# Performance work log

Hardware: AMD Instinct MI355X
Metric: run time of the kernel (lower is better)

The kernel has to match this reference:

```python
import jax, jax.numpy as jnp
import numpy as np

EPS = 1e-8      # torch CosineSimilarity eps (clamps norms)
GAMMA = 0.5
RANK = 2        # hardcoded in the module; rank-1 = 1 negative per sample


def _cos_dist(a, b):
    # angular distance sqrt(2*(1-cos)) along last dim, torch-style eps on norms
    na = jnp.clip(jnp.linalg.norm(a, axis=-1), EPS)
    nb = jnp.clip(jnp.linalg.norm(b, axis=-1), EPS)
    sim = jnp.sum(a * b, axis=-1) / (na * nb)
    return jnp.sqrt(jnp.maximum(2.0 * (1.0 - sim), 1e-12))


def setup_inputs() -> dict:
    key = jax.random.key(0)
    k1, k2, k3 = jax.random.split(key, 3)
    B, D, V = 4096, 512, 50000
    return {
        "input": jax.random.normal(k1, (B, D), dtype=jnp.float32),
        "target": jax.random.normal(k2, (B, D), dtype=jnp.float32),
        "veclist": jax.random.normal(k3, (V, D), dtype=jnp.float32),
    }


def reference(input, target, veclist):
    B = input.shape[0]
    # distance to the true target per sample: [B]
    d_pos = _cos_dist(input, target)

    # brute-force angular kNN over veclist (replaces the Annoy index):
    # max cosine similarity == min angular distance
    inn = input / jnp.clip(jnp.linalg.norm(input, axis=-1, keepdims=True), EPS)
    vnn = veclist / jnp.clip(jnp.linalg.norm(veclist, axis=-1, keepdims=True), EPS)
    sims = inn @ vnn.T                                # [B, V] -- the big GEMM
    _, top_idx = jax.lax.top_k(sims, RANK)            # [B, 2]

    vec0 = veclist[top_idx[:, 0]]                     # [B, D]
    vec1 = veclist[top_idx[:, 1]]                     # [B, D]
    # skip the neighbor if it is exactly the target vector (original `torch.eq` check)
    eq0 = jnp.all(vec0 == target, axis=-1)            # [B]
    neg = jnp.where(eq0[:, None], vec1, vec0)         # [B, D]

    d_neg = _cos_dist(input, neg)                     # [B]
    # original builds sample_dist of shape [rank]=[2] (gamma_vec bug repeats gamma
    # `rank` times), with both entries identical -> sum of positives = 2*relu(margin)
    margin = GAMMA + d_pos - d_neg                    # [B]
    cost = jnp.sum(RANK * jnp.maximum(margin, 0.0))
    return cost / B
```

## Files before the change

### kernel.cpp

```cpp
#include <hip/hip_runtime.h>
#include <hip/hip_bf16.h>
#include <hip/hip_fp8.h>
#include <math.h>

#define B_ROWS 4096
#define DIMS   512
#define V_ROWS 50000
#define V_PAD  50048
#define NTILES 391
#define NT_PAD 392
#define MTILES 32
#define BKB    128
#define NROWS_ALL 54144
#define EPSF   1e-8f
#define QSCALE 64.0f
#define SCALE1 0x7F7F7F7F

typedef float f32x4 __attribute__((ext_vector_type(4)));
typedef int   i32x4 __attribute__((ext_vector_type(4)));
typedef int   i32x8 __attribute__((ext_vector_type(8)));
typedef unsigned long long u64;

__device__ __forceinline__ unsigned int pk4_fp8(float a, float b, float c, float d) {
#if __has_builtin(__builtin_amdgcn_cvt_pk_fp8_f32)
  int w = __builtin_amdgcn_cvt_pk_fp8_f32(a, b, 0, false);
  w = __builtin_amdgcn_cvt_pk_fp8_f32(c, d, w, true);
  return (unsigned int)w;
#else
  __hip_fp8_e4m3 qa(a), qb(b), qc(c), qd(d);
  return (unsigned int)qa.__x | ((unsigned int)qb.__x << 8) |
         ((unsigned int)qc.__x << 16) | ((unsigned int)qd.__x << 24);
#endif
}

__device__ __forceinline__ void lds_load16(const void* g, void* l) {
  __builtin_amdgcn_global_load_lds(
      (const __attribute__((address_space(1))) void*)g,
      (__attribute__((address_space(3))) void*)l, 16, 0, 0);
}

__device__ __forceinline__ u64 pack_key(float v, int col) {
  unsigned int u = __float_as_uint(v);
  unsigned int s = u ^ ((unsigned int)((int)u >> 31) | 0x80000000u);
  return ((u64)s << 32) | (unsigned int)(~col);
}
__device__ __forceinline__ int key_col(u64 k) {
  return (int)(~(unsigned int)k);
}
__device__ __forceinline__ void kmerge(u64& k0, u64& k1, u64 a0, u64 a1) {
  bool bt = a0 > k0;
  u64 lo = bt ? k0 : a0;
  u64 hi = bt ? a1 : k1;
  k0 = bt ? a0 : k0;
  k1 = hi > lo ? hi : lo;
}

__global__ __launch_bounds__(256)
void normalize_rows_kernel(const float* __restrict__ vsrc, const float* __restrict__ isrc,
                           unsigned char* __restrict__ vdst, unsigned char* __restrict__ idst) {
  const int l = threadIdx.x & 63;
  const int gw = (blockIdx.x * 256 + threadIdx.x) >> 6;
  const int nw = (gridDim.x * 256) >> 6;
  for (int row = gw; row < NROWS_ALL; row += nw) {
    const float* src;
    unsigned char* dst;
    if (row < V_PAD) {
      if (row >= V_ROWS) {
        *(uint2*)&vdst[(size_t)row * DIMS + l * 8] = make_uint2(0u, 0u);
        continue;
      }
      src = vsrc + (size_t)row * DIMS;
      dst = vdst + (size_t)row * DIMS;
    } else {
      src = isrc + (size_t)(row - V_PAD) * DIMS;
      dst = idst + (size_t)(row - V_PAD) * DIMS;
    }
    float4 v0 = ((const float4*)src)[l * 2];
    float4 v1 = ((const float4*)src)[l * 2 + 1];
    float ss = v0.x * v0.x + v0.y * v0.y + v0.z * v0.z + v0.w * v0.w
             + v1.x * v1.x + v1.y * v1.y + v1.z * v1.z + v1.w * v1.w;
    #pragma unroll
    for (int d = 1; d < 64; d <<= 1) ss += __shfl_xor(ss, d);
    float s = QSCALE / fmaxf(sqrtf(ss), EPSF);
    uint2 o;
    o.x = pk4_fp8(v0.x * s, v0.y * s, v0.z * s, v0.w * s);
    o.y = pk4_fp8(v1.x * s, v1.y * s, v1.z * s, v1.w * s);
    *(uint2*)&dst[l * 8] = o;
  }
}

__global__ __launch_bounds__(256, 3)
void gemm_top2_kernel(const unsigned char* __restrict__ A8,
                      const unsigned char* __restrict__ B8,
                      ulonglong2* __restrict__ cands) {
  __shared__ __align__(16) unsigned char smem[2 * 128 * BKB];
  unsigned char* const As = smem;
  unsigned char* const Bs = smem + 128 * BKB;

  const int bid = blockIdx.x;
  const int mt = bid & 31;
  const int nt = bid >> 5;
  const int m0 = mt * 128, n0 = nt * 128;

  const int tid = threadIdx.x;
  const int w = tid >> 6, l = tid & 63;
  const int wr = w >> 1, wc = w & 1;
  const int lq = l >> 4, lr = l & 15;
  const int h = lr & 7;

  const int s0 = ((2 * lq) ^ h) * 16;
  const int s1 = ((2 * lq + 1) ^ h) * 16;

  f32x4 acc[4][4] = {};

  for (int k0 = 0; k0 < DIMS; k0 += BKB) {
    #pragma unroll
    for (int it = 0; it < 4; ++it) {
      const int chunk = it * 256 + w * 64 + l;
      const int row = chunk >> 3, c = chunk & 7;
      const int gc = c ^ (row & 7);
      lds_load16(A8 + (size_t)(m0 + row) * DIMS + k0 + gc * 16,
                 &As[(it * 256 + w * 64) * 16]);
      lds_load16(B8 + (size_t)(n0 + row) * DIMS + k0 + gc * 16,
                 &Bs[(it * 256 + w * 64) * 16]);
    }
    __syncthreads();

    i32x8 bf[4];
    #pragma unroll
    for (int tc = 0; tc < 4; ++tc) {
      const int rb = (wc * 64 + tc * 16 + lr) * BKB;
      i32x4 blo = *(const i32x4*)&Bs[rb + s0];
      i32x4 bhi = *(const i32x4*)&Bs[rb + s1];
      bf[tc] = __builtin_shufflevector(blo, bhi, 0, 1, 2, 3, 4, 5, 6, 7);
    }
    #pragma unroll
    for (int tr = 0; tr < 4; ++tr) {
      const int ra = (wr * 64 + tr * 16 + lr) * BKB;
      i32x4 alo = *(const i32x4*)&As[ra + s0];
      i32x4 ahi = *(const i32x4*)&As[ra + s1];
      i32x8 af = __builtin_shufflevector(alo, ahi, 0, 1, 2, 3, 4, 5, 6, 7);
      #pragma unroll
      for (int tc = 0; tc < 4; ++tc)
        acc[tr][tc] = __builtin_amdgcn_mfma_scale_f32_16x16x128_f8f6f4(
            af, bf[tc], acc[tr][tc],
            0, 0,
            0, SCALE1,
            0, SCALE1);
    }
    __syncthreads();
  }

  ulonglong2 (*ep)[32] = (ulonglong2(*)[32])smem;
  const int colbase = n0 + wc * 64 + lr;

  #pragma unroll
  for (int p = 0; p < 2; ++p) {
    #pragma unroll
    for (int trh = 0; trh < 2; ++trh) {
      const int tr = p * 2 + trh;
      #pragma unroll
      for (int rg = 0; rg < 4; ++rg) {
        u64 kk[4];
        #pragma unroll
        for (int tc = 0; tc < 4; ++tc) {
          const int col = colbase + tc * 16;
          const float v = (col < V_ROWS) ? acc[tr][tc][rg] : -INFINITY;
          kk[tc] = pack_key(v, col);
        }
        const bool s01 = kk[0] > kk[1];
        u64 a0 = s01 ? kk[0] : kk[1], a1 = s01 ? kk[1] : kk[0];
        const bool s23 = kk[2] > kk[3];
        u64 b0 = s23 ? kk[2] : kk[3], b1 = s23 ? kk[3] : kk[2];
        kmerge(a0, a1, b0, b1);
        const int slot = wr * 32 + trh * 16 + lq * 4 + rg;
        ep[slot][(wc * 16 + lr) ^ (slot & 7)] = make_ulonglong2(a0, a1);
      }
    }
    __syncthreads();
    {
      const int ms = tid >> 2, q = tid & 3;
      u64 k0 = 0, k1 = 0;
      #pragma unroll
      for (int k = 0; k < 8; ++k) {
        ulonglong2 e = ep[ms][(q * 8 + k) ^ (ms & 7)];
        kmerge(k0, k1, e.x, e.y);
      }
      #pragma unroll
      for (int d = 1; d < 4; d <<= 1) {
        u64 o0 = __shfl_xor(k0, d), o1 = __shfl_xor(k1, d);
        kmerge(k0, k1, o0, o1);
      }
      if (q == 0) {
        const int row = (ms >> 5) * 64 + p * 32 + (ms & 31);
        cands[(size_t)(m0 + row) * NT_PAD + nt] = make_ulonglong2(k0, k1);
      }
    }
    __syncthreads();
  }
}

__global__ __launch_bounds__(256)
void finalize_kernel(const float* __restrict__ input, const float* __restrict__ target,
                     const float* __restrict__ veclist, const ulonglong2* __restrict__ cands,
                     float* __restrict__ contrib) {
  const int b = blockIdx.x;
  const int t = threadIdx.x;
  __shared__ ulonglong2 wpair[4];
  __shared__ int sidx[2];
  __shared__ float red[4][7];
  __shared__ int reda[4];

  u64 k0 = 0, k1 = 0;
  for (int nt = t; nt < NTILES; nt += 256) {
    ulonglong2 c = cands[(size_t)b * NT_PAD + nt];
    kmerge(k0, k1, c.x, c.y);
  }
  #pragma unroll
  for (int d = 1; d < 64; d <<= 1) {
    u64 o0 = __shfl_xor(k0, d), o1 = __shfl_xor(k1, d);
    kmerge(k0, k1, o0, o1);
  }
  if ((t & 63) == 0) wpair[t >> 6] = make_ulonglong2(k0, k1);
  __syncthreads();
  if (t == 0) {
    u64 m0k = wpair[0].x, m1k = wpair[0].y;
    for (int wd = 1; wd < 4; ++wd) kmerge(m0k, m1k, wpair[wd].x, wpair[wd].y);
    sidx[0] = key_col(m0k);
    sidx[1] = key_col(m1k);
  }
  __syncthreads();
  const int idx0 = sidx[0], idx1 = sidx[1];

  const float2* xin = (const float2*)(input  + (size_t)b * DIMS);
  const float2* xtg = (const float2*)(target + (size_t)b * DIMS);
  const float2* xv0 = (const float2*)(veclist + (size_t)idx0 * DIMS);
  const float2* xv1 = (const float2*)(veclist + (size_t)idx1 * DIMS);
  float2 xi = xin[t], tg = xtg[t], a0 = xv0[t], a1 = xv1[t];
  float s[7];
  s[0] = xi.x * xi.x + xi.y * xi.y;
  s[1] = tg.x * tg.x + tg.y * tg.y;
  s[2] = xi.x * tg.x + xi.y * tg.y;
  s[3] = a0.x * a0.x + a0.y * a0.y;
  s[4] = xi.x * a0.x + xi.y * a0.y;
  s[5] = a1.x * a1.x + a1.y * a1.y;
  s[6] = xi.x * a1.x + xi.y * a1.y;
  bool eq = (a0.x == tg.x) && (a0.y == tg.y);
  int weq = __all(eq);
  #pragma unroll
  for (int k = 0; k < 7; ++k)
    #pragma unroll
    for (int d = 1; d < 64; d <<= 1) s[k] += __shfl_xor(s[k], d);
  if ((t & 63) == 0) {
    #pragma unroll
    for (int k = 0; k < 7; ++k) red[t >> 6][k] = s[k];
    reda[t >> 6] = weq;
  }
  __syncthreads();
  if (t == 0) {
    float r[7];
    #pragma unroll
    for (int k = 0; k < 7; ++k)
      r[k] = red[0][k] + red[1][k] + red[2][k] + red[3][k];
    bool eq0 = reda[0] && reda[1] && reda[2] && reda[3];
    float na  = fmaxf(sqrtf(r[0]), EPSF);
    float ntg = fmaxf(sqrtf(r[1]), EPSF);
    float simp = r[2] / (na * ntg);
    float d_pos = sqrtf(fmaxf(2.0f * (1.0f - simp), 1e-12f));
    float nn = eq0 ? fmaxf(sqrtf(r[5]), EPSF) : fmaxf(sqrtf(r[3]), EPSF);
    float dn = eq0 ? r[6] : r[4];
    float simn = dn / (na * nn);
    float d_neg = sqrtf(fmaxf(2.0f * (1.0f - simn), 1e-12f));
    float margin = 0.5f + d_pos - d_neg;
    contrib[b] = 2.0f * fmaxf(margin, 0.0f) * (1.0f / (float)B_ROWS);
  }
}

__global__ __launch_bounds__(256)
void reduce_kernel(const float* __restrict__ contrib, float* __restrict__ out) {
  const int t = threadIdx.x;
  __shared__ float wsum[4];
  float s = 0.0f;
  for (int i = t; i < B_ROWS; i += 256) s += contrib[i];
  #pragma unroll
  for (int d = 1; d < 64; d <<= 1) s += __shfl_xor(s, d);
  if ((t & 63) == 0) wsum[t >> 6] = s;
  __syncthreads();
  if (t == 0) out[0] = wsum[0] + wsum[1] + wsum[2] + wsum[3];
}

extern "C" void kernel_launch(void* const* d_in, const int* in_sizes, int n_in,
                              void* d_out, int out_size, void* d_ws, size_t ws_size,
                              hipStream_t stream) {
  const float* input   = (const float*)d_in[0];
  const float* target  = (const float*)d_in[1];
  const float* veclist = (const float*)d_in[2];
  float* out = (float*)d_out;
  char* ws = (char*)d_ws;
  unsigned char* vnn = (unsigned char*)ws;
  unsigned char* inn = (unsigned char*)(ws + 25624576);
  ulonglong2* cands = (ulonglong2*)(ws + 27721728);
  float* contrib = (float*)(ws + 53411840);

  normalize_rows_kernel<<<2048, 256, 0, stream>>>(veclist, input, vnn, inn);
  gemm_top2_kernel<<<MTILES * NTILES, 256, 0, stream>>>(inn, vnn, cands);
  finalize_kernel<<<B_ROWS, 256, 0, stream>>>(input, target, veclist, cands, contrib);
  reduce_kernel<<<1, 256, 0, stream>>>(contrib, out);
}
```

Before: 362.6 us.

## Double-buffer LDS in FP8 GEMM with explicit waitcnt pipelining and MFMA priority

Turns the GEMM's K loop (four steps of 128) into a fully unrolled, double-buffered LDS pipeline. The next K-slice's global-to-LDS loads are issued before the current slice is computed, with explicit vmcnt waits and raw barriers replacing __syncthreads. MFMA sections are wrapped in s_setprio so the math gets issue priority. LDS use doubles to 64KB and launch bounds drop to 2 blocks per CU, trading occupancy for overlap. The normalize kernel grid size is also doubled.

New measurement: 362.6 us. Within noise of the previous version (+0.0%).

```diff
diff --git a/kernel.cpp b/kernel.cpp
--- a/kernel.cpp
+++ b/kernel.cpp
@@ -89,13 +89,11 @@
   }
 }
 
-__global__ __launch_bounds__(256, 3)
+__global__ __launch_bounds__(256, 2)
 void gemm_top2_kernel(const unsigned char* __restrict__ A8,
                       const unsigned char* __restrict__ B8,
                       ulonglong2* __restrict__ cands) {
-  __shared__ __align__(16) unsigned char smem[2 * 128 * BKB];
-  unsigned char* const As = smem;
-  unsigned char* const Bs = smem + 128 * BKB;
+  __shared__ __align__(16) unsigned char smem[2 * 2 * 128 * BKB];
 
   const int bid = blockIdx.x;
   const int mt = bid & 31;
@@ -113,43 +111,74 @@
 
   f32x4 acc[4][4] = {};
 
-  for (int k0 = 0; k0 < DIMS; k0 += BKB) {
-    #pragma unroll
-    for (int it = 0; it < 4; ++it) {
-      const int chunk = it * 256 + w * 64 + l;
-      const int row = chunk >> 3, c = chunk & 7;
-      const int gc = c ^ (row & 7);
-      lds_load16(A8 + (size_t)(m0 + row) * DIMS + k0 + gc * 16,
-                 &As[(it * 256 + w * 64) * 16]);
-      lds_load16(B8 + (size_t)(n0 + row) * DIMS + k0 + gc * 16,
-                 &Bs[(it * 256 + w * 64) * 16]);
-    }
-    __syncthreads();
-
-    i32x8 bf[4];
-    #pragma unroll
-    for (int tc = 0; tc < 4; ++tc) {
-      const int rb = (wc * 64 + tc * 16 + lr) * BKB;
-      i32x4 blo = *(const i32x4*)&Bs[rb + s0];
-      i32x4 bhi = *(const i32x4*)&Bs[rb + s1];
-      bf[tc] = __builtin_shufflevector(blo, bhi, 0, 1, 2, 3, 4, 5, 6, 7);
-    }
-    #pragma unroll
-    for (int tr = 0; tr < 4; ++tr) {
-      const int ra = (wr * 64 + tr * 16 + lr) * BKB;
-      i32x4 alo = *(const i32x4*)&As[ra + s0];
-      i32x4 ahi = *(const i32x4*)&As[ra + s1];
-      i32x8 af = __builtin_shufflevector(alo, ahi, 0, 1, 2, 3, 4, 5, 6, 7);
-      #pragma unroll
-      for (int tc = 0; tc < 4; ++tc)
-        acc[tr][tc] = __builtin_amdgcn_mfma_scale_f32_16x16x128_f8f6f4(
-            af, bf[tc], acc[tr][tc],
-            0, 0,
-            0, SCALE1,
-            0, SCALE1);
-    }
-    __syncthreads();
-  }
+#define STAGE(buf, k0)                                                        \
+  {                                                                           \
+    unsigned char* Asb = smem + (buf) * 32768;                                \
+    unsigned char* Bsb = Asb + 16384;                                         \
+    _Pragma("unroll")                                                         \
+    for (int it = 0; it < 4; ++it) {                                          \
+      const int chunk = it * 256 + w * 64 + l;                                \
+      const int row = chunk >> 3, c = chunk & 7;                              \
+      const int gc = c ^ (row & 7);                                           \
+      lds_load16(A8 + (size_t)(m0 + row) * DIMS + (k0) + gc * 16,             \
+                 &Asb[(it * 256 + w * 64) * 16]);                             \
+      lds_load16(B8 + (size_t)(n0 + row) * DIMS + (k0) + gc * 16,             \
+                 &Bsb[(it * 256 + w * 64) * 16]);                             \
+    }                                                                         \
+  }
+
+#define COMPUTE(buf)                                                          \
+  {                                                                           \
+    unsigned char* Asb = smem + (buf) * 32768;                                \
+    unsigned char* Bsb = Asb + 16384;                                         \
+    i32x8 bf[4];                                                              \
+    _Pragma("unroll")                                                         \
+    for (int tc = 0; tc < 4; ++tc) {                                          \
+      const int rb = (wc * 64 + tc * 16 + lr) * BKB;                          \
+      i32x4 blo = *(const i32x4*)&Bsb[rb + s0];                               \
+      i32x4 bhi = *(const i32x4*)&Bsb[rb + s1];                               \
+      bf[tc] = __builtin_shufflevector(blo, bhi, 0, 1, 2, 3, 4, 5, 6, 7);     \
+    }                                                                         \
+    _Pragma("unroll")                                                         \
+    for (int tr = 0; tr < 4; ++tr) {                                          \
+      const int ra = (wr * 64 + tr * 16 + lr) * BKB;                          \
+      i32x4 alo = *(const i32x4*)&Asb[ra + s0];                               \
+      i32x4 ahi = *(const i32x4*)&Asb[ra + s1];                               \
+      i32x8 af = __builtin_shufflevector(alo, ahi, 0, 1, 2, 3, 4, 5, 6, 7);   \
+      __builtin_amdgcn_s_setprio(1);                                          \
+      _Pragma("unroll")                                                       \
+      for (int tc = 0; tc < 4; ++tc)                                          \
+        acc[tr][tc] = __builtin_amdgcn_mfma_scale_f32_16x16x128_f8f6f4(       \
+            af, bf[tc], acc[tr][tc], 0, 0, 0, SCALE1, 0, SCALE1);             \
+      __builtin_amdgcn_s_setprio(0);                                          \
+    }                                                                         \
+  }
+
+  STAGE(0, 0);
+  STAGE(1, 128);
+
+  asm volatile("s_waitcnt vmcnt(8)" ::: "memory");
+  __builtin_amdgcn_s_barrier();
+  COMPUTE(0);
+  __builtin_amdgcn_s_barrier();
+  STAGE(0, 256);
+
+  asm volatile("s_waitcnt vmcnt(8)" ::: "memory");
+  __builtin_amdgcn_s_barrier();
+  COMPUTE(1);
+  __builtin_amdgcn_s_barrier();
+  STAGE(1, 384);
+
+  asm volatile("s_waitcnt vmcnt(8)" ::: "memory");
+  __builtin_amdgcn_s_barrier();
+  COMPUTE(0);
+  __builtin_amdgcn_s_barrier();
+
+  asm volatile("s_waitcnt vmcnt(0)" ::: "memory");
+  __builtin_amdgcn_s_barrier();
+  COMPUTE(1);
+#undef STAGE
+#undef COMPUTE
 
   ulonglong2 (*ep)[32] = (ulonglong2(*)[32])smem;
   const int colbase = n0 + wc * 64 + lr;
@@ -302,7 +331,7 @@
   ulonglong2* cands = (ulonglong2*)(ws + 27721728);
   float* contrib = (float*)(ws + 53411840);
 
-  normalize_rows_kernel<<<2048, 256, 0, stream>>>(veclist, input, vnn, inn);
+  normalize_rows_kernel<<<4096, 256, 0, stream>>>(veclist, input, vnn, inn);
   gemm_top2_kernel<<<MTILES * NTILES, 256, 0, stream>>>(inn, vnn, cands);
   finalize_kernel<<<B_ROWS, 256, 0, stream>>>(input, target, veclist, cands, contrib);
   reduce_kernel<<<1, 256, 0, stream>>>(contrib, out);
```

## Load GEMM operands directly from global memory into registers, dropping LDS staging

Applied to the files above, without the earlier changes.

The FP8 GEMM+top2 kernel no longer stages A and B tiles through LDS with global_load_lds and barriers. Each wave now reads its MFMA fragments straight from global memory, and the K loop is fully unrolled. LDS is kept only for the epilogue top-2 merge, and the occupancy hint drops from 3 to 2 blocks. The goal is to remove the LDS round-trip and the barrier stalls, but operand reuse now depends on L1/L2 caches and the global accesses are less coalesced. The normalize kernel grid is also doubled.

New measurement: 574.9 us. +58.6%, slower.

```diff
diff --git a/kernel.cpp b/kernel.cpp
--- a/kernel.cpp
+++ b/kernel.cpp
@@ -10,7 +10,6 @@
 #define NTILES 391
 #define NT_PAD 392
 #define MTILES 32
-#define BKB    128
 #define NROWS_ALL 54144
 #define EPSF   1e-8f
 #define QSCALE 64.0f
@@ -31,12 +30,6 @@
   return (unsigned int)qa.__x | ((unsigned int)qb.__x << 8) |
          ((unsigned int)qc.__x << 16) | ((unsigned int)qd.__x << 24);
 #endif
-}
-
-__device__ __forceinline__ void lds_load16(const void* g, void* l) {
-  __builtin_amdgcn_global_load_lds(
-      (const __attribute__((address_space(1))) void*)g,
-      (__attribute__((address_space(3))) void*)l, 16, 0, 0);
 }
 
 __device__ __forceinline__ u64 pack_key(float v, int col) {
@@ -89,13 +82,11 @@
   }
 }
 
-__global__ __launch_bounds__(256, 3)
+__global__ __launch_bounds__(256, 2)
 void gemm_top2_kernel(const unsigned char* __restrict__ A8,
                       const unsigned char* __restrict__ B8,
                       ulonglong2* __restrict__ cands) {
-  __shared__ __align__(16) unsigned char smem[2 * 128 * BKB];
-  unsigned char* const As = smem;
-  unsigned char* const Bs = smem + 128 * BKB;
+  __shared__ __align__(16) ulonglong2 ep[64][32];
 
   const int bid = blockIdx.x;
   const int mt = bid & 31;
@@ -106,39 +97,31 @@
   const int w = tid >> 6, l = tid & 63;
   const int wr = w >> 1, wc = w & 1;
   const int lq = l >> 4, lr = l & 15;
-  const int h = lr & 7;
-
-  const int s0 = ((2 * lq) ^ h) * 16;
-  const int s1 = ((2 * lq + 1) ^ h) * 16;
+
+  const unsigned char* abase[4];
+  const unsigned char* bbase[4];
+  #pragma unroll
+  for (int tr = 0; tr < 4; ++tr)
+    abase[tr] = A8 + (size_t)(m0 + wr * 64 + tr * 16 + lr) * DIMS + lq * 16;
+  #pragma unroll
+  for (int tc = 0; tc < 4; ++tc)
+    bbase[tc] = B8 + (size_t)(n0 + wc * 64 + tc * 16 + lr) * DIMS + lq * 16;
 
   f32x4 acc[4][4] = {};
 
-  for (int k0 = 0; k0 < DIMS; k0 += BKB) {
-    #pragma unroll
-    for (int it = 0; it < 4; ++it) {
-      const int chunk = it * 256 + w * 64 + l;
-      const int row = chunk >> 3, c = chunk & 7;
-      const int gc = c ^ (row & 7);
-      lds_load16(A8 + (size_t)(m0 + row) * DIMS + k0 + gc * 16,
-                 &As[(it * 256 + w * 64) * 16]);
-      lds_load16(B8 + (size_t)(n0 + row) * DIMS + k0 + gc * 16,
-                 &Bs[(it * 256 + w * 64) * 16]);
-    }
-    __syncthreads();
-
+  #pragma unroll
+  for (int k0 = 0; k0 < DIMS; k0 += 128) {
     i32x8 bf[4];
     #pragma unroll
     for (int tc = 0; tc < 4; ++tc) {
-      const int rb = (wc * 64 + tc * 16 + lr) * BKB;
-      i32x4 blo = *(const i32x4*)&Bs[rb + s0];
-      i32x4 bhi = *(const i32x4*)&Bs[rb + s1];
+      i32x4 blo = *(const i32x4*)(bbase[tc] + k0);
+      i32x4 bhi = *(const i32x4*)(bbase[tc] + k0 + 64);
       bf[tc] = __builtin_shufflevector(blo, bhi, 0, 1, 2, 3, 4, 5, 6, 7);
     }
     #pragma unroll
     for (int tr = 0; tr < 4; ++tr) {
-      const int ra = (wr * 64 + tr * 16 + lr) * BKB;
-      i32x4 alo = *(const i32x4*)&As[ra + s0];
-      i32x4 ahi = *(const i32x4*)&As[ra + s1];
+      i32x4 alo = *(const i32x4*)(abase[tr] + k0);
+      i32x4 ahi = *(const i32x4*)(abase[tr] + k0 + 64);
       i32x8 af = __builtin_shufflevector(alo, ahi, 0, 1, 2, 3, 4, 5, 6, 7);
       #pragma unroll
       for (int tc = 0; tc < 4; ++tc)
@@ -148,10 +131,8 @@
             0, SCALE1,
             0, SCALE1);
     }
-    __syncthreads();
-  }
-
-  ulonglong2 (*ep)[32] = (ulonglong2(*)[32])smem;
+  }
+
   const int colbase = n0 + wc * 64 + lr;
 
   #pragma unroll
@@ -302,7 +283,7 @@
   ulonglong2* cands = (ulonglong2*)(ws + 27721728);
   float* contrib = (float*)(ws + 53411840);
 
-  normalize_rows_kernel<<<2048, 256, 0, stream>>>(veclist, input, vnn, inn);
+  normalize_rows_kernel<<<4096, 256, 0, stream>>>(veclist, input, vnn, inn);
   gemm_top2_kernel<<<MTILES * NTILES, 256, 0, stream>>>(inn, vnn, cands);
   finalize_kernel<<<B_ROWS, 256, 0, stream>>>(input, target, veclist, cands, contrib);
   reduce_kernel<<<1, 256, 0, stream>>>(contrib, out);
```

## Pre-pack A operand in MFMA fragment order and load it directly into registers

Applied to the files above, without the earlier changes.

The normalize kernel now writes the quantized input rows in a pre-swizzled layout that matches the MFMA fragment order, so the GEMM loads A fragments straight from global memory into registers with coalesced 16-byte loads and never stages them in LDS. This removes the A tile from shared memory, halving LDS traffic and staging per K step, and the epilogue now gets its own LDS buffer. In exchange A is read from global/L2 by each wave without LDS sharing, and register pressure rises. The normalize grid size is also doubled.

New measurement: 362.5 us. Within noise of the previous version (-0.0%).

```diff
diff --git a/kernel.cpp b/kernel.cpp
--- a/kernel.cpp
+++ b/kernel.cpp
@@ -10,7 +10,6 @@
 #define NTILES 391
 #define NT_PAD 392
 #define MTILES 32
-#define BKB    128
 #define NROWS_ALL 54144
 #define EPSF   1e-8f
 #define QSCALE 64.0f
@@ -57,23 +56,20 @@
 
 __global__ __launch_bounds__(256)
 void normalize_rows_kernel(const float* __restrict__ vsrc, const float* __restrict__ isrc,
-                           unsigned char* __restrict__ vdst, unsigned char* __restrict__ idst) {
+                           unsigned char* __restrict__ vdst, unsigned char* __restrict__ apk) {
   const int l = threadIdx.x & 63;
   const int gw = (blockIdx.x * 256 + threadIdx.x) >> 6;
   const int nw = (gridDim.x * 256) >> 6;
   for (int row = gw; row < NROWS_ALL; row += nw) {
     const float* src;
-    unsigned char* dst;
     if (row < V_PAD) {
       if (row >= V_ROWS) {
         *(uint2*)&vdst[(size_t)row * DIMS + l * 8] = make_uint2(0u, 0u);
         continue;
       }
       src = vsrc + (size_t)row * DIMS;
-      dst = vdst + (size_t)row * DIMS;
     } else {
       src = isrc + (size_t)(row - V_PAD) * DIMS;
-      dst = idst + (size_t)(row - V_PAD) * DIMS;
     }
     float4 v0 = ((const float4*)src)[l * 2];
     float4 v1 = ((const float4*)src)[l * 2 + 1];
@@ -85,17 +81,24 @@
     uint2 o;
     o.x = pk4_fp8(v0.x * s, v0.y * s, v0.z * s, v0.w * s);
     o.y = pk4_fp8(v1.x * s, v1.y * s, v1.z * s, v1.w * s);
-    *(uint2*)&dst[l * 8] = o;
+    if (row < V_PAD) {
+      *(uint2*)&vdst[(size_t)row * DIMS + l * 8] = o;
+    } else {
+      const int m = row - V_PAD;
+      const int rec = (((( (m >> 7) * 2 + ((m >> 6) & 1) ) * 4 + (l >> 4)) * 4
+                        + ((m >> 4) & 3)) * 2 + ((l >> 1) & 1));
+      const int off = rec * 1024 + (((l >> 2) & 3) * 16 + (m & 15)) * 16 + (l & 1) * 8;
+      *(uint2*)&apk[off] = o;
+    }
   }
 }
 
 __global__ __launch_bounds__(256, 3)
-void gemm_top2_kernel(const unsigned char* __restrict__ A8,
+void gemm_top2_kernel(const unsigned char* __restrict__ Apk,
                       const unsigned char* __restrict__ B8,
                       ulonglong2* __restrict__ cands) {
-  __shared__ __align__(16) unsigned char smem[2 * 128 * BKB];
-  unsigned char* const As = smem;
-  unsigned char* const Bs = smem + 128 * BKB;
+  __shared__ __align__(16) unsigned char Bs[128 * 128];
+  __shared__ __align__(16) ulonglong2 ep[64][32];
 
   const int bid = blockIdx.x;
   const int mt = bid & 31;
@@ -111,35 +114,40 @@
   const int s0 = ((2 * lq) ^ h) * 16;
   const int s1 = ((2 * lq + 1) ^ h) * 16;
 
+  const unsigned char* const Abase =
+      Apk + (size_t)(mt * 2 + wr) * 32768 + l * 16;
+
   f32x4 acc[4][4] = {};
 
-  for (int k0 = 0; k0 < DIMS; k0 += BKB) {
+  for (int ks = 0; ks < 4; ++ks) {
     #pragma unroll
     for (int it = 0; it < 4; ++it) {
       const int chunk = it * 256 + w * 64 + l;
       const int row = chunk >> 3, c = chunk & 7;
       const int gc = c ^ (row & 7);
-      lds_load16(A8 + (size_t)(m0 + row) * DIMS + k0 + gc * 16,
-                 &As[(it * 256 + w * 64) * 16]);
-      lds_load16(B8 + (size_t)(n0 + row) * DIMS + k0 + gc * 16,
+      lds_load16(B8 + (size_t)(n0 + row) * DIMS + ks * 128 + gc * 16,
                  &Bs[(it * 256 + w * 64) * 16]);
     }
+    i32x4 areg[4][2];
+    #pragma unroll
+    for (int tr = 0; tr < 4; ++tr) {
+      areg[tr][0] = *(const i32x4*)(Abase + ks * 8192 + tr * 2048);
+      areg[tr][1] = *(const i32x4*)(Abase + ks * 8192 + tr * 2048 + 1024);
+    }
     __syncthreads();
 
     i32x8 bf[4];
     #pragma unroll
     for (int tc = 0; tc < 4; ++tc) {
-      const int rb = (wc * 64 + tc * 16 + lr) * BKB;
+      const int rb = (wc * 64 + tc * 16 + lr) * 128;
       i32x4 blo = *(const i32x4*)&Bs[rb + s0];
       i32x4 bhi = *(const i32x4*)&Bs[rb + s1];
       bf[tc] = __builtin_shufflevector(blo, bhi, 0, 1, 2, 3, 4, 5, 6, 7);
     }
     #pragma unroll
     for (int tr = 0; tr < 4; ++tr) {
-      const int ra = (wr * 64 + tr * 16 + lr) * BKB;
-      i32x4 alo = *(const i32x4*)&As[ra + s0];
-      i32x4 ahi = *(const i32x4*)&As[ra + s1];
-      i32x8 af = __builtin_shufflevector(alo, ahi, 0, 1, 2, 3, 4, 5, 6, 7);
+      i32x8 af = __builtin_shufflevector(areg[tr][0], areg[tr][1],
+                                         0, 1, 2, 3, 4, 5, 6, 7);
       #pragma unroll
       for (int tc = 0; tc < 4; ++tc)
         acc[tr][tc] = __builtin_amdgcn_mfma_scale_f32_16x16x128_f8f6f4(
@@ -151,7 +159,6 @@
     __syncthreads();
   }
 
-  ulonglong2 (*ep)[32] = (ulonglong2(*)[32])smem;
   const int colbase = n0 + wc * 64 + lr;
 
   #pragma unroll
@@ -298,12 +305,12 @@
   float* out = (float*)d_out;
   char* ws = (char*)d_ws;
   unsigned char* vnn = (unsigned char*)ws;
-  unsigned char* inn = (unsigned char*)(ws + 25624576);
+  unsigned char* apk = (unsigned char*)(ws + 25624576);
   ulonglong2* cands = (ulonglong2*)(ws + 27721728);
   float* contrib = (float*)(ws + 53411840);
 
-  normalize_rows_kernel<<<2048, 256, 0, stream>>>(veclist, input, vnn, inn);
-  gemm_top2_kernel<<<MTILES * NTILES, 256, 0, stream>>>(inn, vnn, cands);
+  normalize_rows_kernel<<<4096, 256, 0, stream>>>(veclist, input, vnn, apk);
+  gemm_top2_kernel<<<MTILES * NTILES, 256, 0, stream>>>(apk, vnn, cands);
   finalize_kernel<<<B_ROWS, 256, 0, stream>>>(input, target, veclist, cands, contrib);
   reduce_kernel<<<1, 256, 0, stream>>>(contrib, out);
 }
```
